# Kernel optimization log

Measured on AMD Instinct MI355X. Metric: run time of the kernel, lower is better.

Reference implementation:

```python
import jax, jax.numpy as jnp
import numpy as np

DIM = 512
NL = 4
P = 8
B = 4
L = 8192  # byte-level sequence length
LP = L // P  # patch-level sequence length


def _ln(x, g, b, eps=1e-5):
    m = jnp.mean(x, axis=-1, keepdims=True)
    v = jnp.mean((x - m) ** 2, axis=-1, keepdims=True)
    return (x - m) * jax.lax.rsqrt(v + eps) * g + b


def setup_inputs() -> dict:
    key = jax.random.key(0)
    ks = jax.random.split(key, 24)
    s = 0.02
    inp = {
        "bytes_in": jax.random.randint(ks[0], (B, L), 0, 256, dtype=jnp.int32),
        "byte_emb": jax.random.normal(ks[1], (256, DIM), jnp.float32) * s,
        # patch encoder Conv1d(kernel=stride=P): weight laid out [P, D_in, D_out]
        "enc_w": jax.random.normal(ks[2], (P, DIM, DIM), jnp.float32) * s,
        "enc_b": jnp.zeros((DIM,), jnp.float32),
        "hash_proj": jax.random.normal(ks[3], (DIM, DIM), jnp.float32) * s,
        # per-layer stacked params
        "qkv_w": jax.random.normal(ks[4], (NL, DIM, 3 * DIM), jnp.float32) * s,
        "qkv_b": jnp.zeros((NL, 3 * DIM), jnp.float32),
        "gate_w": jax.random.normal(ks[5], (NL, DIM, DIM), jnp.float32) * s,
        "gate_b": jnp.zeros((NL, DIM), jnp.float32),
        "ln1_g": jnp.ones((NL, DIM), jnp.float32),
        "ln1_b": jnp.zeros((NL, DIM), jnp.float32),
        "mlp_w1": jax.random.normal(ks[6], (NL, DIM, 4 * DIM), jnp.float32) * s,
        "mlp_b1": jnp.zeros((NL, 4 * DIM), jnp.float32),
        "mlp_w2": jax.random.normal(ks[7], (NL, 4 * DIM, DIM), jnp.float32) * s,
        "mlp_b2": jnp.zeros((NL, DIM), jnp.float32),
        "ln2_g": jnp.ones((NL, DIM), jnp.float32),
        "ln2_b": jnp.zeros((NL, DIM), jnp.float32),
        # patch decoder ConvTranspose1d(kernel=stride=P): weight [D_in, P, D_out]
        "dec_w": jax.random.normal(ks[8], (DIM, P, DIM), jnp.float32) * s,
        "dec_b": jnp.zeros((DIM,), jnp.float32),
        "head_w": jax.random.normal(ks[9], (DIM, 256), jnp.float32) * s,
        "head_b": jnp.zeros((256,), jnp.float32),
    }
    return inp


def reference(bytes_in, byte_emb, enc_w, enc_b, hash_proj,
              qkv_w, qkv_b, gate_w, gate_b, ln1_g, ln1_b,
              mlp_w1, mlp_b1, mlp_w2, mlp_b2, ln2_g, ln2_b,
              dec_w, dec_b, head_w, head_b):
    # byte embedding: [B, L, D]
    x = byte_emb[bytes_in]
    # non-overlapping Conv1d(kernel=stride=P) == patch-wise contraction
    xp = x.reshape(B, LP, P, DIM)
    x = jnp.einsum('blpd,pdo->blo', xp, enc_w) + enc_b  # [B, LP, D]
    # hash projection
    x = x + jnp.tanh(x @ hash_proj)
    for i in range(NL):
        # LinearLatentKernel
        h = _ln(x, ln1_g[i], ln1_b[i])
        qkv = h @ qkv_w[i] + qkv_b[i]
        q, k, v = jnp.split(qkv, 3, axis=-1)
        kv_state = jnp.cumsum(k * v, axis=1)
        g = jax.nn.sigmoid(h @ gate_w[i] + gate_b[i])
        x = x + q * kv_state * g
        # MLP
        h = _ln(x, ln2_g[i], ln2_b[i])
        h = jax.nn.gelu(h @ mlp_w1[i] + mlp_b1[i], approximate=False)
        x = x + h @ mlp_w2[i] + mlp_b2[i]
    # ConvTranspose1d(kernel=stride=P): each patch expands to P positions
    y = jnp.einsum('bld,dpo->blpo', x, dec_w).reshape(B, L, DIM) + dec_b
    logits = y @ head_w + head_b  # [B, L, 256]
    return logits
```

## Files before the change

### kernel.cpp

```cpp
#include <hip/hip_runtime.h>
#include <hip/hip_bf16.h>
#include <math.h>

#define DIMD 512
#define NLAYER 4
#define PP 8
#define BBATCH 4
#define LBYTES 8192
#define LPATCH 1024
#define MROWS (BBATCH * LPATCH)

#define NCHUNK 64
#define CLEN   16
#define QGS    (4 * DIMD)

typedef __bf16 bf16x8 __attribute__((ext_vector_type(8)));
typedef float f32x4 __attribute__((ext_vector_type(4)));
typedef unsigned short u16x4 __attribute__((ext_vector_type(4)));
typedef unsigned short u16x8 __attribute__((ext_vector_type(8)));

__device__ __forceinline__ unsigned short f2bf(float f) {
    union { float f; unsigned u; } v; v.f = f;
    unsigned r = v.u + 0x7FFFu + ((v.u >> 16) & 1u);
    return (unsigned short)(r >> 16);
}
__device__ __forceinline__ float bf2f(unsigned short u) {
    union { unsigned u; float f; } v; v.u = ((unsigned)u) << 16;
    return v.f;
}

__device__ __forceinline__ void glds16(const unsigned short* g, unsigned short* l) {
    __builtin_amdgcn_global_load_lds((__attribute__((address_space(1))) void*)g,
                                     (__attribute__((address_space(3))) void*)l,
                                     16, 0, 0);
}

template<int TM, int ACT, bool BIAS, bool RES, bool OBF>
__global__ __launch_bounds__(256)
void mfma_gemm(const unsigned short* __restrict__ A, int lda, long aZ,
               const unsigned short* __restrict__ Bt, int ldb, long bZ,
               const float* __restrict__ bias,
               const float* __restrict__ res, int ldr,
               void* __restrict__ Cv, int ldc, long cZ, int K)
{
    constexpr int M_REP = TM / 32;
    __shared__ unsigned short As[TM * 32];
    __shared__ unsigned short Bs[128 * 32];

    const int tid = threadIdx.x;
    const int w = tid >> 6, l = tid & 63;
    const int row0 = blockIdx.x * TM;
    const int col0 = blockIdx.y * 128;
    A  += (size_t)blockIdx.z * aZ;
    Bt += (size_t)blockIdx.z * bZ;
    unsigned short* Cb = (unsigned short*)Cv + (size_t)blockIdx.z * cZ;
    float*          Cf = (float*)Cv          + (size_t)blockIdx.z * cZ;

    const int cA = w * 64 + l;
    const unsigned short* gA0 = A + (size_t)(row0 + (cA >> 2)) * lda + (cA & 3) * 8;
    const unsigned short* gB0 = Bt + (size_t)(col0 + (cA >> 2)) * ldb + (cA & 3) * 8;
    const unsigned short* gB1 = Bt + (size_t)(col0 + 64 + (cA >> 2)) * ldb + (cA & 3) * 8;
    unsigned short* lA0 = &As[w * 512];
    unsigned short* lB0 = &Bs[w * 512];
    unsigned short* lB1 = &Bs[2048 + w * 512];
    const unsigned short* gA1 = nullptr;
    unsigned short* lA1 = nullptr;
    if constexpr (TM == 128) {
        gA1 = A + (size_t)(row0 + 64 + (cA >> 2)) * lda + (cA & 3) * 8;
        lA1 = &As[2048 + w * 512];
    }

    const int wr = (w >> 1) * (TM / 2);
    const int wc = (w & 1) * 64;
    const int lr = l & 15, lk = (l >> 4) * 8;
    const int aBase = (wr + lr) * 32 + lk;
    const int bBase = (wc + lr) * 32 + lk;

    f32x4 acc[M_REP][4] = {};

    for (int k0 = 0; k0 < K; k0 += 32) {
        glds16(gA0, lA0);  gA0 += 32;
        if constexpr (TM == 128) { glds16(gA1, lA1); gA1 += 32; }
        glds16(gB0, lB0);  gB0 += 32;
        glds16(gB1, lB1);  gB1 += 32;
        __syncthreads();
        bf16x8 af[M_REP], bfr[4];
        #pragma unroll
        for (int m = 0; m < M_REP; m++)
            af[m] = *reinterpret_cast<const bf16x8*>(&As[aBase + m * 512]);
        #pragma unroll
        for (int n = 0; n < 4; n++)
            bfr[n] = *reinterpret_cast<const bf16x8*>(&Bs[bBase + n * 512]);
        #pragma unroll
        for (int m = 0; m < M_REP; m++)
            #pragma unroll
            for (int n = 0; n < 4; n++)
                acc[m][n] = __builtin_amdgcn_mfma_f32_16x16x32_bf16(
                    af[m], bfr[n], acc[m][n], 0, 0, 0);
        __syncthreads();
    }

    const int r0 = row0 + wr + (l >> 4) * 4;
    const int c0 = col0 + wc + lr;
    float bv[4] = {0.f, 0.f, 0.f, 0.f};
    if (BIAS) {
        #pragma unroll
        for (int n = 0; n < 4; n++) bv[n] = bias[c0 + n * 16];
    }
    #pragma unroll
    for (int m = 0; m < M_REP; m++) {
        #pragma unroll
        for (int j = 0; j < 4; j++) {
            const int row = r0 + m * 16 + j;
            #pragma unroll
            for (int n = 0; n < 4; n++) {
                float v = acc[m][n][j];
                if (BIAS) v += bv[n];
                if (ACT == 1) v = tanhf(v);
                if (ACT == 2) v = 0.5f * v * (1.f + erff(v * 0.70710678118f));
                if (RES) v += res[(size_t)row * ldr + c0 + n * 16];
                if (OBF) Cb[(size_t)row * ldc + c0 + n * 16] = f2bf(v);
                else     Cf[(size_t)row * ldc + c0 + n * 16] = v;
            }
        }
    }
}

__device__ __forceinline__ void packT_body(float* sm, const float* __restrict__ in,
                                           unsigned short* __restrict__ out,
                                           int K, int N, int bx, int by)
{
    float (*t)[33] = (float(*)[33])sm;
    const int k0 = bx * 32, n0 = by * 32;
    const int tx = threadIdx.x & 31, ty = threadIdx.x >> 5;
    #pragma unroll
    for (int i = 0; i < 4; i++)
        t[ty + i * 8][tx] = in[(size_t)(k0 + ty + i * 8) * N + n0 + tx];
    __syncthreads();
    #pragma unroll
    for (int i = 0; i < 4; i++)
        out[(size_t)(n0 + ty + i * 8) * K + k0 + tx] = f2bf(t[tx][ty + i * 8]);
}

__device__ __forceinline__ void cast_body(const float* __restrict__ in,
                                          unsigned short* __restrict__ out, int blk)
{
    const long i = ((long)blk * 256 + threadIdx.x) * 8;
    float4 a = *(const float4*)(in + i);
    float4 b = *(const float4*)(in + i + 4);
    u16x8 o;
    o[0] = f2bf(a.x); o[1] = f2bf(a.y); o[2] = f2bf(a.z); o[3] = f2bf(a.w);
    o[4] = f2bf(b.x); o[5] = f2bf(b.y); o[6] = f2bf(b.z); o[7] = f2bf(b.w);
    *reinterpret_cast<u16x8*>(out + i) = o;
}

__global__ __launch_bounds__(256)
void megapack(const float* __restrict__ qkv_w, const float* __restrict__ gate_w,
              const float* __restrict__ mlp_w1, const float* __restrict__ mlp_w2,
              const float* __restrict__ hash_proj, const float* __restrict__ head_w,
              const float* __restrict__ enc_w, const float* __restrict__ dec_w,
              const float* __restrict__ byte_emb,
              const float* __restrict__ qkv_b, const float* __restrict__ gate_b,
              unsigned short* __restrict__ wcat, unsigned short* __restrict__ w1T,
              unsigned short* __restrict__ w2T, unsigned short* __restrict__ whashT,
              unsigned short* __restrict__ hwT, unsigned short* __restrict__ encT,
              unsigned short* __restrict__ decb, unsigned short* __restrict__ embB,
              float* __restrict__ cbias)
{
    __shared__ float sm[32 * 33];
    int id = blockIdx.x;
    if (id < 3072) {
        int z = id / 768, r = id % 768;
        packT_body(sm, qkv_w + (size_t)z * 512 * 1536, wcat + (size_t)z * 2048 * 512,
                   512, 1536, r % 16, r / 16);
    } else if (id < 4096) {
        id -= 3072; int z = id / 256, r = id % 256;
        packT_body(sm, gate_w + (size_t)z * 512 * 512,
                   wcat + (size_t)z * 2048 * 512 + (size_t)1536 * 512,
                   512, 512, r % 16, r / 16);
    } else if (id < 8192) {
        id -= 4096; int z = id / 1024, r = id % 1024;
        packT_body(sm, mlp_w1 + (size_t)z * 512 * 2048, w1T + (size_t)z * 2048 * 512,
                   512, 2048, r % 16, r / 16);
    } else if (id < 12288) {
        id -= 8192; int z = id / 1024, r = id % 1024;
        packT_body(sm, mlp_w2 + (size_t)z * 2048 * 512, w2T + (size_t)z * 512 * 2048,
                   2048, 512, r % 64, r / 64);
    } else if (id < 12544) {
        id -= 12288;
        packT_body(sm, hash_proj, whashT, 512, 512, id % 16, id / 16);
    } else if (id < 12672) {
        id -= 12544;
        packT_body(sm, head_w, hwT, 512, 256, id % 16, id / 16);
    } else if (id < 14720) {
        id -= 12672; int z = id / 256, r = id % 256;
        packT_body(sm, enc_w + (size_t)z * 512 * 512, encT + (size_t)z * 512 * 512,
                   512, 512, r % 16, r / 16);
    } else if (id < 15744) {
        cast_body(dec_w, decb, id - 14720);
    } else if (id < 15808) {
        cast_body(byte_emb, embB, id - 15744);
    } else {
        id -= 15808;
        const int i = id >> 3;
        const int n = (id & 7) * 256 + threadIdx.x;
        cbias[i * 2048 + n] = (n < 1536) ? qkv_b[i * 1536 + n] : gate_b[i * 512 + n - 1536];
    }
}

__global__ __launch_bounds__(256)
void ln_kernel(const float* __restrict__ x, const float* __restrict__ g,
               const float* __restrict__ b, unsigned short* __restrict__ h)
{
    const int row = blockIdx.x * 4 + (threadIdx.x >> 6);
    const int lane = threadIdx.x & 63;
    const float* xr = x + (long)row * DIMD;
    float4 v0 = *(const float4*)(xr + lane * 8);
    float4 v1 = *(const float4*)(xr + lane * 8 + 4);
    float xv[8] = {v0.x, v0.y, v0.z, v0.w, v1.x, v1.y, v1.z, v1.w};
    float s = 0.f, q = 0.f;
    #pragma unroll
    for (int j = 0; j < 8; j++) { s += xv[j]; q += xv[j] * xv[j]; }
    #pragma unroll
    for (int off = 1; off < 64; off <<= 1) {
        s += __shfl_xor(s, off);
        q += __shfl_xor(q, off);
    }
    const float mean = s * (1.f / DIMD);
    const float var  = q * (1.f / DIMD) - mean * mean;
    const float rstd = rsqrtf(var + 1e-5f);
    float4 g0 = *(const float4*)(g + lane * 8);
    float4 g1 = *(const float4*)(g + lane * 8 + 4);
    float4 b0 = *(const float4*)(b + lane * 8);
    float4 b1 = *(const float4*)(b + lane * 8 + 4);
    float gv[8] = {g0.x, g0.y, g0.z, g0.w, g1.x, g1.y, g1.z, g1.w};
    float bb[8] = {b0.x, b0.y, b0.z, b0.w, b1.x, b1.y, b1.z, b1.w};
    u16x8 o;
    #pragma unroll
    for (int j = 0; j < 8; j++) o[j] = f2bf((xv[j] - mean) * rstd * gv[j] + bb[j]);
    *reinterpret_cast<u16x8*>(h + (long)row * DIMD + lane * 8) = o;
}

__global__ __launch_bounds__(128)
void embed_kernel(const int* __restrict__ bytes, const float* __restrict__ E,
                  const float* __restrict__ enc_b, float* __restrict__ x0,
                  unsigned short* __restrict__ x0b)
{
    const int patch = blockIdx.x;
    __shared__ int by[PP];
    if (threadIdx.x < PP) by[threadIdx.x] = bytes[patch * PP + threadIdx.x];
    __syncthreads();
    const int o = threadIdx.x * 4;
    float4 acc = *(const float4*)(enc_b + o);
    #pragma unroll
    for (int p = 0; p < PP; p++) {
        float4 e = *(const float4*)(E + ((long)(p * 256 + by[p])) * DIMD + o);
        acc.x += e.x; acc.y += e.y; acc.z += e.z; acc.w += e.w;
    }
    *(float4*)(x0 + (long)patch * DIMD + o) = acc;
    u16x4 ob; ob[0] = f2bf(acc.x); ob[1] = f2bf(acc.y);
    ob[2] = f2bf(acc.z); ob[3] = f2bf(acc.w);
    *reinterpret_cast<u16x4*>(x0b + (long)patch * DIMD + o) = ob;
}

__global__ __launch_bounds__(256)
void scan_partial(const unsigned short* __restrict__ qg, float* __restrict__ S)
{
    const int b = blockIdx.x >> 6, c = blockIdx.x & 63, d2 = threadIdx.x * 2;
    const unsigned short* base = qg + (size_t)(b * LPATCH + c * CLEN) * QGS;
    float s0 = 0.f, s1 = 0.f;
    for (int l = 0; l < CLEN; l++) {
        ushort2 kk = *(const ushort2*)(base + l * QGS + DIMD + d2);
        ushort2 vv = *(const ushort2*)(base + l * QGS + 2 * DIMD + d2);
        s0 = fmaf(bf2f(kk.x), bf2f(vv.x), s0);
        s1 = fmaf(bf2f(kk.y), bf2f(vv.y), s1);
    }
    *(float2*)(S + (size_t)(b * NCHUNK + c) * DIMD + d2) = make_float2(s0, s1);
}

__global__ __launch_bounds__(256)
void scan_apply_ln(const unsigned short* __restrict__ qg,
                   const float* __restrict__ S, float* __restrict__ x,
                   const float* __restrict__ lg, const float* __restrict__ lb,
                   unsigned short* __restrict__ h)
{
    const int b = blockIdx.x >> 6, c = blockIdx.x & 63;
    const int t = threadIdx.x, d2 = t * 2;
    const int wid = t >> 6, lane = t & 63;

    float kv0 = 0.f, kv1 = 0.f;
    const float* Sb = S + (size_t)b * NCHUNK * DIMD;
    for (int j = 0; j < c; j++) {
        float2 sv = *(const float2*)(Sb + j * DIMD + d2);
        kv0 += sv.x; kv1 += sv.y;
    }
    const float g0 = lg[d2], g1 = lg[d2 + 1];
    const float b0 = lb[d2], b1 = lb[d2 + 1];
    const int row0 = b * LPATCH + c * CLEN;
    __shared__ float redS[4], redQ[4];

    for (int l = 0; l < CLEN; l++) {
        const unsigned short* qb = qg + (size_t)(row0 + l) * QGS;
        ushort2 qq = *(const ushort2*)(qb + d2);
        ushort2 kk = *(const ushort2*)(qb + DIMD + d2);
        ushort2 vv = *(const ushort2*)(qb + 2 * DIMD + d2);
        ushort2 gg = *(const ushort2*)(qb + 3 * DIMD + d2);
        kv0 = fmaf(bf2f(kk.x), bf2f(vv.x), kv0);
        kv1 = fmaf(bf2f(kk.y), bf2f(vv.y), kv1);
        const float sg0 = 1.f / (1.f + expf(-bf2f(gg.x)));
        const float sg1 = 1.f / (1.f + expf(-bf2f(gg.y)));
        float* xr = x + (size_t)(row0 + l) * DIMD;
        float2 xv = *(const float2*)(xr + d2);
        const float n0 = xv.x + bf2f(qq.x) * kv0 * sg0;
        const float n1 = xv.y + bf2f(qq.y) * kv1 * sg1;
        *(float2*)(xr + d2) = make_float2(n0, n1);

        float s = n0 + n1, qs = n0 * n0 + n1 * n1;
        #pragma unroll
        for (int off = 1; off < 64; off <<= 1) {
            s += __shfl_xor(s, off); qs += __shfl_xor(qs, off);
        }
        if (lane == 0) { redS[wid] = s; redQ[wid] = qs; }
        __syncthreads();
        const float ts = redS[0] + redS[1] + redS[2] + redS[3];
        const float tq = redQ[0] + redQ[1] + redQ[2] + redQ[3];
        __syncthreads();
        const float mean = ts * (1.f / DIMD);
        const float var  = tq * (1.f / DIMD) - mean * mean;
        const float rstd = rsqrtf(var + 1e-5f);
        ushort2 ho;
        ho.x = f2bf((n0 - mean) * rstd * g0 + b0);
        ho.y = f2bf((n1 - mean) * rstd * g1 + b1);
        *(ushort2*)(h + (size_t)(row0 + l) * DIMD + d2) = ho;
    }
}

__global__ __launch_bounds__(256)
void fbias2(const unsigned short* __restrict__ hwT, const float* __restrict__ dec_b,
            const float* __restrict__ head_b, float* __restrict__ fb)
{
    const int w = threadIdx.x >> 6, l = threadIdx.x & 63;
    const int o = blockIdx.x * 4 + w;
    u16x8 hv = *reinterpret_cast<const u16x8*>(hwT + (size_t)o * DIMD + l * 8);
    float4 d0 = *(const float4*)(dec_b + l * 8);
    float4 d1 = *(const float4*)(dec_b + l * 8 + 4);
    float dd[8] = {d0.x, d0.y, d0.z, d0.w, d1.x, d1.y, d1.z, d1.w};
    float s = 0.f;
    #pragma unroll
    for (int j = 0; j < 8; j++) s += bf2f(hv[j]) * dd[j];
    #pragma unroll
    for (int off = 1; off < 64; off <<= 1) s += __shfl_xor(s, off);
    if (l == 0) {
        float v = s + head_b[o];
        #pragma unroll
        for (int p = 0; p < PP; p++) fb[p * 256 + o] = v;
    }
}

extern "C" void kernel_launch(void* const* d_in, const int* in_sizes, int n_in,
                              void* d_out, int out_size, void* d_ws, size_t ws_size,
                              hipStream_t stream)
{
    (void)in_sizes; (void)n_in; (void)out_size; (void)ws_size;

    const int*   bytes_in  = (const int*)d_in[0];
    const float* byte_emb  = (const float*)d_in[1];
    const float* enc_w     = (const float*)d_in[2];
    const float* enc_b     = (const float*)d_in[3];
    const float* hash_proj = (const float*)d_in[4];
    const float* qkv_w     = (const float*)d_in[5];
    const float* qkv_b     = (const float*)d_in[6];
    const float* gate_w    = (const float*)d_in[7];
    const float* gate_b    = (const float*)d_in[8];
    const float* ln1_g     = (const float*)d_in[9];
    const float* ln1_b     = (const float*)d_in[10];
    const float* mlp_w1    = (const float*)d_in[11];
    const float* mlp_b1    = (const float*)d_in[12];
    const float* mlp_w2    = (const float*)d_in[13];
    const float* mlp_b2    = (const float*)d_in[14];
    const float* ln2_g     = (const float*)d_in[15];
    const float* ln2_b     = (const float*)d_in[16];
    const float* dec_w     = (const float*)d_in[17];
    const float* dec_b     = (const float*)d_in[18];
    const float* head_w    = (const float*)d_in[19];
    const float* head_b    = (const float*)d_in[20];
    float* out = (float*)d_out;

    char* ws = (char*)d_ws;
    size_t o = 0;
    auto alloc = [&](size_t bytes) { char* p = ws + o; o += (bytes + 255) & ~(size_t)255; return p; };
    unsigned short* wcat   = (unsigned short*)alloc((size_t)4 * 2048 * 512 * 2);
    unsigned short* w1T    = (unsigned short*)alloc((size_t)4 * 2048 * 512 * 2);
    unsigned short* w2T    = (unsigned short*)alloc((size_t)4 * 512 * 2048 * 2);
    unsigned short* whashT = (unsigned short*)alloc((size_t)512 * 512 * 2);
    unsigned short* wWfT   = (unsigned short*)alloc((size_t)2048 * 512 * 2);
    unsigned short* encT   = (unsigned short*)alloc((size_t)8 * 512 * 512 * 2);
    unsigned short* hwT    = (unsigned short*)alloc((size_t)256 * 512 * 2);
    unsigned short* decb   = (unsigned short*)alloc((size_t)512 * 8 * 512 * 2);
    unsigned short* embB   = (unsigned short*)alloc((size_t)256 * 512 * 2);
    float* cbias           = (float*)alloc((size_t)4 * 2048 * 4);
    float* fb              = (float*)alloc(2048 * 4);
    float* E               = (float*)alloc((size_t)8 * 256 * 512 * 4);
    float* x               = (float*)alloc((size_t)MROWS * DIMD * 4);
    float* x0              = (float*)alloc((size_t)MROWS * DIMD * 4);
    unsigned short* x0b    = (unsigned short*)alloc((size_t)MROWS * DIMD * 2);
    unsigned short* h      = (unsigned short*)alloc((size_t)MROWS * DIMD * 2);
    unsigned short* xb     = (unsigned short*)alloc((size_t)MROWS * DIMD * 2);
    float* S               = (float*)alloc((size_t)BBATCH * NCHUNK * DIMD * 4);
    unsigned short* qg     = (unsigned short*)alloc((size_t)MROWS * 2048 * 2);
    unsigned short* hid    = (unsigned short*)alloc((size_t)MROWS * 2048 * 2);

    megapack<<<dim3(15840), 256, 0, stream>>>(
        qkv_w, gate_w, mlp_w1, mlp_w2, hash_proj, head_w, enc_w, dec_w, byte_emb,
        qkv_b, gate_b,
        wcat, w1T, w2T, whashT, hwT, encT, decb, embB, cbias);

    mfma_gemm<64, 0, false, false, true><<<dim3(4, 4, 8), 256, 0, stream>>>(
        hwT, 512, 0L, decb, PP * 512, 512L,
        nullptr, nullptr, 0, wWfT, 512, (long)256 * 512, 512);
    fbias2<<<dim3(64), 256, 0, stream>>>(hwT, dec_b, head_b, fb);

    mfma_gemm<64, 0, false, false, false><<<dim3(4, 4, 8), 256, 0, stream>>>(
        embB, 512, 0L, encT, 512, (long)512 * 512,
        nullptr, nullptr, 0, E, 512, (long)256 * 512, 512);

    embed_kernel<<<dim3(MROWS), dim3(128), 0, stream>>>(bytes_in, E, enc_b, x0, x0b);

    mfma_gemm<64, 1, false, true, false><<<dim3(MROWS / 64, 4, 1), 256, 0, stream>>>(
        x0b, DIMD, 0L, whashT, DIMD, 0L, nullptr, x0, DIMD, x, DIMD, 0L, DIMD);

    for (int i = 0; i < NLAYER; i++) {
        ln_kernel<<<dim3(MROWS / 4), 256, 0, stream>>>(x, ln1_g + i * DIMD, ln1_b + i * DIMD, h);
        mfma_gemm<128, 0, true, false, true><<<dim3(MROWS / 128, 16, 1), 256, 0, stream>>>(
            h, DIMD, 0L, wcat + (size_t)i * 2048 * 512, DIMD, 0L,
            cbias + (size_t)i * 2048, nullptr, 0, qg, 2048, 0L, DIMD);
        scan_partial<<<dim3(BBATCH * NCHUNK), 256, 0, stream>>>(qg, S);
        scan_apply_ln<<<dim3(BBATCH * NCHUNK), 256, 0, stream>>>(
            qg, S, x, ln2_g + i * DIMD, ln2_b + i * DIMD, h);
        mfma_gemm<128, 2, true, false, true><<<dim3(MROWS / 128, 16, 1), 256, 0, stream>>>(
            h, DIMD, 0L, w1T + (size_t)i * 2048 * 512, DIMD, 0L,
            mlp_b1 + (size_t)i * 2048, nullptr, 0, hid, 2048, 0L, DIMD);
        if (i < NLAYER - 1) {
            mfma_gemm<64, 0, true, true, false><<<dim3(MROWS / 64, 4, 1), 256, 0, stream>>>(
                hid, 2048, 0L, w2T + (size_t)i * 512 * 2048, 2048, 0L,
                mlp_b2 + (size_t)i * DIMD, x, DIMD, x, DIMD, 0L, 2048);
        } else {
            mfma_gemm<64, 0, true, true, true><<<dim3(MROWS / 64, 4, 1), 256, 0, stream>>>(
                hid, 2048, 0L, w2T + (size_t)i * 512 * 2048, 2048, 0L,
                mlp_b2 + (size_t)i * DIMD, x, DIMD, xb, DIMD, 0L, 2048);
        }
    }

    mfma_gemm<128, 0, true, false, false><<<dim3(MROWS / 128, 16, 1), 256, 0, stream>>>(
        xb, DIMD, 0L, wWfT, DIMD, 0L, fb, nullptr, 0, out, 2048, 0L, DIMD);
}
```

Baseline: 531.3 us.

## Split scan-apply-LN into prefix scan, apply, and separate LayerNorm kernels

Replaces the fused scan_apply_ln kernel with three kernels: a small prefix-sum kernel over chunk partial sums, a scan_apply kernel that updates x with no block-wide reductions, and the existing ln_kernel for the second LayerNorm. This removes the quadratic per-block reload of earlier chunk sums and the two __syncthreads per row inside the serial 16-row loop. In exchange it adds two launches per layer, a prefix kernel using only 4 blocks, and an extra round trip of x through global memory for the separate LayerNorm.

```diff
diff --git a/kernel.cpp b/kernel.cpp
--- a/kernel.cpp
+++ b/kernel.cpp
@@ -278,60 +278,41 @@
     *(float2*)(S + (size_t)(b * NCHUNK + c) * DIMD + d2) = make_float2(s0, s1);
 }
 
-__global__ __launch_bounds__(256)
-void scan_apply_ln(const unsigned short* __restrict__ qg,
-                   const float* __restrict__ S, float* __restrict__ x,
-                   const float* __restrict__ lg, const float* __restrict__ lb,
-                   unsigned short* __restrict__ h)
-{
-    const int b = blockIdx.x >> 6, c = blockIdx.x & 63;
-    const int t = threadIdx.x, d2 = t * 2;
-    const int wid = t >> 6, lane = t & 63;
-
-    float kv0 = 0.f, kv1 = 0.f;
-    const float* Sb = S + (size_t)b * NCHUNK * DIMD;
-    for (int j = 0; j < c; j++) {
-        float2 sv = *(const float2*)(Sb + j * DIMD + d2);
-        kv0 += sv.x; kv1 += sv.y;
-    }
-    const float g0 = lg[d2], g1 = lg[d2 + 1];
-    const float b0 = lb[d2], b1 = lb[d2 + 1];
+__global__ __launch_bounds__(512)
+void scan_prefix(float* __restrict__ S)
+{
+    const int b = blockIdx.x, d = threadIdx.x;
+    float run = 0.f;
+    #pragma unroll 4
+    for (int c = 0; c < NCHUNK; c++) {
+        float v = S[(b * NCHUNK + c) * DIMD + d];
+        S[(b * NCHUNK + c) * DIMD + d] = run;
+        run += v;
+    }
+}
+
+__global__ __launch_bounds__(256)
+void scan_apply(const unsigned short* __restrict__ qg,
+                const float* __restrict__ S, float* __restrict__ x)
+{
+    const int b = blockIdx.x >> 6, c = blockIdx.x & 63, d2 = threadIdx.x * 2;
+    float2 kv = *(const float2*)(S + (size_t)(b * NCHUNK + c) * DIMD + d2);
     const int row0 = b * LPATCH + c * CLEN;
-    __shared__ float redS[4], redQ[4];
-
     for (int l = 0; l < CLEN; l++) {
         const unsigned short* qb = qg + (size_t)(row0 + l) * QGS;
         ushort2 qq = *(const ushort2*)(qb + d2);
         ushort2 kk = *(const ushort2*)(qb + DIMD + d2);
         ushort2 vv = *(const ushort2*)(qb + 2 * DIMD + d2);
         ushort2 gg = *(const ushort2*)(qb + 3 * DIMD + d2);
-        kv0 = fmaf(bf2f(kk.x), bf2f(vv.x), kv0);
-        kv1 = fmaf(bf2f(kk.y), bf2f(vv.y), kv1);
+        kv.x = fmaf(bf2f(kk.x), bf2f(vv.x), kv.x);
+        kv.y = fmaf(bf2f(kk.y), bf2f(vv.y), kv.y);
         const float sg0 = 1.f / (1.f + expf(-bf2f(gg.x)));
         const float sg1 = 1.f / (1.f + expf(-bf2f(gg.y)));
         float* xr = x + (size_t)(row0 + l) * DIMD;
         float2 xv = *(const float2*)(xr + d2);
-        const float n0 = xv.x + bf2f(qq.x) * kv0 * sg0;
-        const float n1 = xv.y + bf2f(qq.y) * kv1 * sg1;
-        *(float2*)(xr + d2) = make_float2(n0, n1);
-
-        float s = n0 + n1, qs = n0 * n0 + n1 * n1;
-        #pragma unroll
-        for (int off = 1; off < 64; off <<= 1) {
-            s += __shfl_xor(s, off); qs += __shfl_xor(qs, off);
-        }
-        if (lane == 0) { redS[wid] = s; redQ[wid] = qs; }
-        __syncthreads();
-        const float ts = redS[0] + redS[1] + redS[2] + redS[3];
-        const float tq = redQ[0] + redQ[1] + redQ[2] + redQ[3];
-        __syncthreads();
-        const float mean = ts * (1.f / DIMD);
-        const float var  = tq * (1.f / DIMD) - mean * mean;
-        const float rstd = rsqrtf(var + 1e-5f);
-        ushort2 ho;
-        ho.x = f2bf((n0 - mean) * rstd * g0 + b0);
-        ho.y = f2bf((n1 - mean) * rstd * g1 + b1);
-        *(ushort2*)(h + (size_t)(row0 + l) * DIMD + d2) = ho;
+        xv.x += bf2f(qq.x) * kv.x * sg0;
+        xv.y += bf2f(qq.y) * kv.y * sg1;
+        *(float2*)(xr + d2) = xv;
     }
 }
 
@@ -435,8 +416,9 @@
             h, DIMD, 0L, wcat + (size_t)i * 2048 * 512, DIMD, 0L,
             cbias + (size_t)i * 2048, nullptr, 0, qg, 2048, 0L, DIMD);
         scan_partial<<<dim3(BBATCH * NCHUNK), 256, 0, stream>>>(qg, S);
-        scan_apply_ln<<<dim3(BBATCH * NCHUNK), 256, 0, stream>>>(
-            qg, S, x, ln2_g + i * DIMD, ln2_b + i * DIMD, h);
+        scan_prefix<<<dim3(BBATCH), dim3(512), 0, stream>>>(S);
+        scan_apply<<<dim3(BBATCH * NCHUNK), 256, 0, stream>>>(qg, S, x);
+        ln_kernel<<<dim3(MROWS / 4), 256, 0, stream>>>(x, ln2_g + i * DIMD, ln2_b + i * DIMD, h);
         mfma_gemm<128, 2, true, false, true><<<dim3(MROWS / 128, 16, 1), 256, 0, stream>>>(
             h, DIMD, 0L, w1T + (size_t)i * 2048 * 512, DIMD, 0L,
             mlp_b1 + (size_t)i * 2048, nullptr, 0, hid, 2048, 0L, DIMD);
```

Result: faster. 479.5 us (-9.8%).
